# Performance work log

Hardware: AMD Instinct MI355X
Metric: run time of the kernel (lower is better)

The kernel has to match this reference:

```python
import jax, jax.numpy as jnp
import numpy as np

B, S, HID, NH = 4, 2048, 1024, 16
DH = HID // NH  # 64
SCALE = 1.0 / float(np.sqrt(DH))


def _linear_params(key, scale=0.02):
    kw, kb = jax.random.split(key)
    W = jax.random.normal(kw, (HID, HID), dtype=jnp.float32) * scale
    b = jax.random.normal(kb, (HID,), dtype=jnp.float32) * scale
    return W, b


def setup_inputs() -> dict:
    key = jax.random.key(0)
    ks = jax.random.split(key, 9)
    x = jax.random.normal(ks[0], (B, S, HID), dtype=jnp.float32)
    reasoning_mask = jax.random.uniform(ks[1], (B, S, 1, 1), dtype=jnp.float32)
    Wq, bq = _linear_params(ks[2])
    Wk, bk = _linear_params(ks[3])
    Wv, bv = _linear_params(ks[4])
    Wqr, bqr = _linear_params(ks[5])
    Wkr, bkr = _linear_params(ks[6])
    Wo, bo = _linear_params(ks[7])
    return {"x": x, "reasoning_mask": reasoning_mask,
            "Wq": Wq, "bq": bq, "Wk": Wk, "bk": bk, "Wv": Wv, "bv": bv,
            "Wqr": Wqr, "bqr": bqr, "Wkr": Wkr, "bkr": bkr, "Wo": Wo, "bo": bo}


def reference(x, reasoning_mask, Wq, bq, Wk, bk, Wv, bv, Wqr, bqr, Wkr, bkr, Wo, bo):
    # Projections: x @ W + b, then view (B, S, NH, DH)
    def proj(W, b):
        return (jnp.einsum('bsh,hd->bsd', x, W) + b).reshape(B, S, NH, DH)

    q = proj(Wq, bq)
    k = proj(Wk, bk)
    v = proj(Wv, bv)
    q_r = proj(Wqr, bqr)
    k_r = proj(Wkr, bkr)

    # Reasoning-gated blend of standard and reasoning projections
    q = q * (1.0 - reasoning_mask) + q_r * reasoning_mask
    k = k * (1.0 - reasoning_mask) + k_r * reasoning_mask

    # Faithful to source: matmul over the LAST two dims of (B,S,NH,DH),
    # i.e. per-token attention ACROSS HEADS -> scores shape (B,S,NH,NH)
    scores = jnp.einsum('bshd,bsed->bshe', q, k) * SCALE
    attn = jax.nn.softmax(scores, axis=-1)  # dropout is identity at eval
    out = jnp.einsum('bshe,bsed->bshd', attn, v)  # (B,S,NH,DH)

    # Faithful transpose(1,2) + contiguous view to (B, S, HID)
    out = jnp.transpose(out, (0, 2, 1, 3)).reshape(B, -1, HID)
    return jnp.einsum('bsh,hd->bsd', out, Wo) + bo
```

## Files before the change

### kernel.cpp

```cpp
#include <hip/hip_runtime.h>
#include <hip/hip_bf16.h>


typedef __attribute__((ext_vector_type(8))) short short8;
typedef __attribute__((ext_vector_type(4))) short short4v;
typedef __attribute__((ext_vector_type(4))) float f32x4;

#define HID 1024
#define NTOK 8192
#define WT_ELEMS (1024 * 1024)

__device__ __forceinline__ short f2bs(float f) {
  __hip_bfloat16 h = __float2bfloat16(f);
  return *reinterpret_cast<short*>(&h);
}
__device__ __forceinline__ float bs2f(short s) {
  __hip_bfloat16 h;
  *reinterpret_cast<short*>(&h) = s;
  return __bfloat162float(h);
}
__device__ __forceinline__ void gload16(const void* g, void* l) {
  __builtin_amdgcn_global_load_lds(
      (const __attribute__((address_space(1))) void*)g,
      (__attribute__((address_space(3))) void*)l, 16, 0, 0);
}

#define BAR() asm volatile("s_barrier" ::: "memory")
#define VMWAIT(N) asm volatile("s_waitcnt vmcnt(" #N ")" ::: "memory")
#define LGKM0 do { asm volatile("s_waitcnt lgkmcnt(0)" ::: "memory"); \
                   __builtin_amdgcn_sched_barrier(0); } while (0)
#define SCB __builtin_amdgcn_sched_barrier(0)
#define PRIO1 __builtin_amdgcn_s_setprio(1)
#define PRIO0 __builtin_amdgcn_s_setprio(0)
#define MFMA16x16 __builtin_amdgcn_mfma_f32_16x16x32_bf16

__global__ __launch_bounds__(256) void prep_kernel(
    const float* __restrict__ W0, const float* __restrict__ W1,
    const float* __restrict__ W2, const float* __restrict__ W3,
    const float* __restrict__ W4, const float* __restrict__ W5,
    const float* __restrict__ X, short* __restrict__ WT, short* __restrict__ XB)
{
  __shared__ short sT[64][68];
  const int bid = blockIdx.x, tid = threadIdx.x;
  if (bid < 1536) {
    const int z = bid >> 8, rem = bid & 255;
    const float* W = z == 0 ? W0 : z == 1 ? W1 : z == 2 ? W2 : z == 3 ? W3
                   : z == 4 ? W4 : W5;
    short* OUT = WT + (size_t)z * WT_ELEMS;
    const int k0 = (rem & 15) * 64, n0 = (rem >> 4) * 64;
    #pragma unroll
    for (int i = 0; i < 4; i++) {
      const int li = tid + i * 256;
      const int kr = li >> 4, c4 = (li & 15) << 2;
      const f32x4 wv = *reinterpret_cast<const f32x4*>(&W[(size_t)(k0 + kr) * HID + n0 + c4]);
      short4v s4;
      #pragma unroll
      for (int j = 0; j < 4; j++) s4[j] = f2bs(wv[j]);
      *reinterpret_cast<short4v*>(&sT[kr][c4]) = s4;
    }
    __syncthreads();
    #pragma unroll
    for (int i = 0; i < 4; i++) {
      const int li = tid + i * 256;
      const int nr = li >> 4, k4 = (li & 15) << 2;
      short4v o;
      #pragma unroll
      for (int j = 0; j < 4; j++) o[j] = sT[k4 + j][nr];
      const int kcol = (k0 + k4) ^ ((nr & 7) << 3);
      *reinterpret_cast<short4v*>(&OUT[(size_t)(n0 + nr) * HID + kcol]) = o;
    }
  } else {
    const int gid = (bid - 1536) * 256 + tid;
    const int row = gid >> 7, kc = (gid & 127) << 3;
    const f32x4 a = *reinterpret_cast<const f32x4*>(&X[(size_t)row * HID + kc]);
    const f32x4 b = *reinterpret_cast<const f32x4*>(&X[(size_t)row * HID + kc + 4]);
    short8 s;
    #pragma unroll
    for (int j = 0; j < 4; j++) { s[j] = f2bs(a[j]); s[4 + j] = f2bs(b[j]); }
    const int phys = (kc & ~63) | ((kc & 63) ^ ((row & 7) << 3));
    *reinterpret_cast<short8*>(&XB[(size_t)row * HID + phys]) = s;
  }
}

__global__ __launch_bounds__(512, 2) void gated8_kernel(
    const short* __restrict__ XB, const short* __restrict__ WTbase,
    const float* __restrict__ bq, const float* __restrict__ bqr,
    const float* __restrict__ bk, const float* __restrict__ bkr,
    const float* __restrict__ MASK,
    __hip_bfloat16* __restrict__ qg, __hip_bfloat16* __restrict__ kg)
{
  __shared__ short lA[2][256][64];
  __shared__ short lB1[2][128][64];
  __shared__ short lB2[2][128][64];

  const int d = blockIdx.x;
  const int bx = d & 31, byz = d >> 5;
  const int by = byz & 7, z = byz >> 3;

  const short* W1T = WTbase + (size_t)(2 * z) * WT_ELEMS;
  const short* W2T = W1T + WT_ELEMS;
  const float* B1b = z ? bk : bq;
  const float* B2b = z ? bkr : bqr;
  __hip_bfloat16* OUT = z ? kg : qg;

  const int m0 = bx * 256, n0 = by * 128;
  const int tid = threadIdx.x, lane = tid & 63, w = tid >> 6;
  const int wr = (w >> 1) * 64, wc = (w & 1) * 64;
  const int lrow = lane & 15, lkhi = (lane >> 4) << 3;
  const int swz = (lrow & 7) << 3;
  const int srow = lane >> 3, scol = (lane & 7) << 3;

  f32x4 acc1[4][4] = {}, acc2[4][4] = {};
  short8 bf1k[4], bf2k[4];
  short8 afA0, afA1, afA2, afA3;
  short8 afB0, afB1, afB2, afB3;

  auto stA2 = [&](int slot, int kt, int i0) {
    const int k0 = kt * 64;
    #pragma unroll
    for (int i = 0; i < 2; i++) {
      const int chunk = w * 4 + i0 + i;
      gload16(&XB[(size_t)(m0 + chunk * 8 + srow) * HID + k0 + scol],
              &lA[slot][chunk * 8][0]);
    }
  };
  auto stB1s = [&](int slot, int kt) {
    const int k0 = kt * 64;
    #pragma unroll
    for (int i = 0; i < 2; i++) {
      const int chunk = w * 2 + i;
      gload16(&W1T[(size_t)(n0 + chunk * 8 + srow) * HID + k0 + scol],
              &lB1[slot][chunk * 8][0]);
    }
  };
  auto stB2s = [&](int slot, int kt) {
    const int k0 = kt * 64;
    #pragma unroll
    for (int i = 0; i < 2; i++) {
      const int chunk = w * 2 + i;
      gload16(&W2T[(size_t)(n0 + chunk * 8 + srow) * HID + k0 + scol],
              &lB2[slot][chunk * 8][0]);
    }
  };
  auto rdA = [&](int s, int m, int kk) -> short8 {
    const int lk = (kk * 32 + lkhi) ^ swz;
    return *reinterpret_cast<const short8*>(&lA[s][wr + m * 16 + lrow][lk]);
  };

#define RDB1(S, KK)                                                                   \
  _Pragma("unroll")                                                                   \
  for (int n = 0; n < 4; n++) {                                                       \
    const int lk = ((KK) * 32 + lkhi) ^ swz;                                          \
    bf1k[n] = *reinterpret_cast<const short8*>(&lB1[S][wc + n * 16 + lrow][lk]);      \
  }
#define RDB2(S, KK)                                                                   \
  _Pragma("unroll")                                                                   \
  for (int n = 0; n < 4; n++) {                                                       \
    const int lk = ((KK) * 32 + lkhi) ^ swz;                                          \
    bf2k[n] = *reinterpret_cast<const short8*>(&lB2[S][wc + n * 16 + lrow][lk]);      \
  }
#define MM16A(A0, A1, A2, A3)                                             \
  _Pragma("unroll")                                                       \
  for (int n = 0; n < 4; n++) {                                           \
    acc1[0][n] = MFMA16x16(A0, bf1k[n], acc1[0][n], 0, 0, 0);             \
    acc1[1][n] = MFMA16x16(A1, bf1k[n], acc1[1][n], 0, 0, 0);             \
    acc1[2][n] = MFMA16x16(A2, bf1k[n], acc1[2][n], 0, 0, 0);             \
    acc1[3][n] = MFMA16x16(A3, bf1k[n], acc1[3][n], 0, 0, 0);             \
  }
#define MM16B(A0, A1, A2, A3)                                             \
  _Pragma("unroll")                                                       \
  for (int n = 0; n < 4; n++) {                                           \
    acc2[0][n] = MFMA16x16(A0, bf2k[n], acc2[0][n], 0, 0, 0);             \
    acc2[1][n] = MFMA16x16(A1, bf2k[n], acc2[1][n], 0, 0, 0);             \
    acc2[2][n] = MFMA16x16(A2, bf2k[n], acc2[2][n], 0, 0, 0);             \
    acc2[3][n] = MFMA16x16(A3, bf2k[n], acc2[3][n], 0, 0, 0);             \
  }
#define GTILE(S, SN, TS)                                                 \
                                                                 \
  afA0 = rdA(S, 0, 0); afA1 = rdA(S, 1, 0);                              \
  afA2 = rdA(S, 2, 0); afA3 = rdA(S, 3, 0);                              \
  RDB1(S, 0);                                                            \
  stA2(SN, TS, 0); stA2(SN, TS, 2);                                      \
  BAR(); LGKM0;                                                          \
  PRIO1; MM16A(afA0, afA1, afA2, afA3) PRIO0; SCB;                       \
  VMWAIT(4);                                                             \
  BAR();                                                                 \
                                                                 \
  RDB2(S, 0);                                                            \
  stB1s(SN, TS); stB2s(SN, TS);                                          \
  BAR(); LGKM0;                                                          \
  PRIO1; MM16B(afA0, afA1, afA2, afA3) PRIO0; SCB;                       \
  BAR();                                                                 \
                                                                 \
  afB0 = rdA(S, 0, 1); afB1 = rdA(S, 1, 1);                              \
  afB2 = rdA(S, 2, 1); afB3 = rdA(S, 3, 1);                              \
  RDB1(S, 1);                                                            \
  BAR(); LGKM0;                                                          \
  PRIO1; MM16A(afB0, afB1, afB2, afB3) PRIO0; SCB;                       \
  BAR();                                                                 \
                                                                 \
  RDB2(S, 1);                                                            \
  BAR(); LGKM0;                                                          \
  PRIO1; MM16B(afB0, afB1, afB2, afB3) PRIO0; SCB;                       \
  VMWAIT(2);                                                             \
  BAR();

  stA2(0, 0, 0); stA2(0, 0, 2); stB1s(0, 0); stB2s(0, 0);
  VMWAIT(2);
  BAR();

  #pragma unroll 1
  for (int i = 0; i < 16; i++) {
    const int S = i & 1, SN = S ^ 1;
    const int TS = (i < 15) ? i + 1 : 15;
    GTILE(S, SN, TS)
  }
  VMWAIT(0);
#undef GTILE
#undef MM16A
#undef MM16B
#undef RDB1
#undef RDB2

  #pragma unroll
  for (int m = 0; m < 4; m++) {
    const int rbase = m0 + wr + m * 16 + ((lane >> 4) << 2);
    #pragma unroll
    for (int n = 0; n < 4; n++) {
      const int col = n0 + wc + n * 16 + lrow;
      const float bias1 = B1b[col];
      const float bias2 = B2b[col];
      #pragma unroll
      for (int r = 0; r < 4; r++) {
        const int row = rbase + r;
        const float mk = MASK[row];
        const float val = (acc1[m][n][r] + bias1) * (1.f - mk) +
                          (acc2[m][n][r] + bias2) * mk;
        OUT[(size_t)row * HID + col] = __float2bfloat16(val);
      }
    }
  }
}

template<bool OUTF32>
__global__ __launch_bounds__(512, 2) void plain8_kernel(
    const short* __restrict__ A, const short* __restrict__ WT,
    const float* __restrict__ BIAS, void* __restrict__ OUTv)
{
  __shared__ short lA[3][256][64];
  __shared__ short lB[3][128][64];

  const int d = blockIdx.x;
  const int bx = d & 31, by = d >> 5;

  const int m0 = bx * 256, n0 = by * 128;
  const int tid = threadIdx.x, lane = tid & 63, w = tid >> 6;
  const int wr = (w >> 1) * 64, wc = (w & 1) * 64;
  const int lrow = lane & 15, lkhi = (lane >> 4) << 3;
  const int swz = (lrow & 7) << 3;
  const int srow = lane >> 3, scol = (lane & 7) << 3;

  f32x4 acc[4][4] = {};
  short8 paf[2][4], pbf[2][4];

  auto stTrip = [&](int slot, int kt, int t) {
    const int k0 = kt * 64;
    if (t == 0) {
      #pragma unroll
      for (int i = 0; i < 3; i++) {
        const int chunk = w * 4 + i;
        gload16(&A[(size_t)(m0 + chunk * 8 + srow) * HID + k0 + scol],
                &lA[slot][chunk * 8][0]);
      }
    } else {
      const int chunk = w * 4 + 3;
      gload16(&A[(size_t)(m0 + chunk * 8 + srow) * HID + k0 + scol],
              &lA[slot][chunk * 8][0]);
      #pragma unroll
      for (int i = 0; i < 2; i++) {
        const int bchunk = w * 2 + i;
        gload16(&WT[(size_t)(n0 + bchunk * 8 + srow) * HID + k0 + scol],
                &lB[slot][bchunk * 8][0]);
      }
    }
  };

#define RDP(S, KK)                                                                    \
  _Pragma("unroll")                                                                   \
  for (int m = 0; m < 4; m++) {                                                       \
    const int lk = ((KK) * 32 + lkhi) ^ swz;                                          \
    paf[KK][m] = *reinterpret_cast<const short8*>(&lA[S][wr + m * 16 + lrow][lk]);    \
    pbf[KK][m] = *reinterpret_cast<const short8*>(&lB[S][wc + m * 16 + lrow][lk]);    \
  }
#define PMM16(KK)                                                                     \
  _Pragma("unroll")                                                                   \
  for (int m = 0; m < 4; m++)                                                         \
    _Pragma("unroll")                                                                 \
    for (int n = 0; n < 4; n++)                                                       \
      acc[m][n] = MFMA16x16(paf[KK][m], pbf[KK][n], acc[m][n], 0, 0, 0);

  stTrip(0, 0, 0); stTrip(0, 0, 1);
  stTrip(1, 1, 0); stTrip(1, 1, 1);
  VMWAIT(6);
  BAR();

  int s = 0, s2 = 2;
  #pragma unroll 1
  for (int t = 0; t < 16; t++) {
    const int TS = (t < 14) ? t + 2 : 15;
    RDP(s, 0)
    stTrip(s2, TS, 0);
    BAR(); LGKM0;
    PRIO1; PMM16(0) PRIO0; SCB;
    BAR();
    RDP(s, 1)
    stTrip(s2, TS, 1);
    BAR(); LGKM0;
    PRIO1; PMM16(1) PRIO0; SCB;
    VMWAIT(6);
    BAR();
    s = (s == 2) ? 0 : s + 1;
    s2 = (s2 == 2) ? 0 : s2 + 1;
  }
  VMWAIT(0);
#undef PMM16
#undef RDP

  #pragma unroll
  for (int m = 0; m < 4; m++) {
    const int rbase = m0 + wr + m * 16 + ((lane >> 4) << 2);
    #pragma unroll
    for (int n = 0; n < 4; n++) {
      const int col = n0 + wc + n * 16 + lrow;
      const float bias = BIAS[col];
      #pragma unroll
      for (int r = 0; r < 4; r++) {
        const float val = acc[m][n][r] + bias;
        const size_t oidx = (size_t)(rbase + r) * HID + col;
        if (OUTF32) ((float*)OUTv)[oidx] = val;
        else ((__hip_bfloat16*)OUTv)[oidx] = __float2bfloat16(val);
      }
    }
  }
}

__global__ __launch_bounds__(256) void attn_kernel(
    const __hip_bfloat16* __restrict__ Q, const __hip_bfloat16* __restrict__ K,
    const __hip_bfloat16* __restrict__ V, __hip_bfloat16* __restrict__ O)
{
  const int t = blockIdx.x;
  const int b = t >> 11, s = t & 2047;
  __shared__ float sQ[16][68], sK[16][68], sV[16][68];
  __shared__ float sA[16][17];
  const int tid = threadIdx.x;
  const size_t tb = (size_t)t * HID;

  {
    const int h = tid >> 4, d0 = (tid & 15) << 2;
    const int o = (h << 6) + d0;
    const short4v qv = *reinterpret_cast<const short4v*>(&((const short*)Q)[tb + o]);
    const short4v kv = *reinterpret_cast<const short4v*>(&((const short*)K)[tb + o]);
    const short4v vv = *reinterpret_cast<const short4v*>(&((const short*)V)[tb + o]);
    #pragma unroll
    for (int j = 0; j < 4; j++) {
      sQ[h][d0 + j] = bs2f(qv[j]);
      sK[h][d0 + j] = bs2f(kv[j]);
      sV[h][d0 + j] = bs2f(vv[j]);
    }
  }
  __syncthreads();

  const int h = tid >> 4, e = tid & 15;
  float sc = 0.f;
  #pragma unroll
  for (int dd = 0; dd < 64; dd++) sc += sQ[h][dd] * sK[e][dd];
  sc *= 0.125f;

  float mx = sc;
  mx = fmaxf(mx, __shfl_xor(mx, 1));
  mx = fmaxf(mx, __shfl_xor(mx, 2));
  mx = fmaxf(mx, __shfl_xor(mx, 4));
  mx = fmaxf(mx, __shfl_xor(mx, 8));
  const float p = __expf(sc - mx);
  float sm = p;
  sm += __shfl_xor(sm, 1);
  sm += __shfl_xor(sm, 2);
  sm += __shfl_xor(sm, 4);
  sm += __shfl_xor(sm, 8);
  sA[h][e] = p / sm;
  __syncthreads();

  const int row7 = (s >> 4) & 7;
  const size_t ob = ((size_t)b * 2048 + (s >> 4)) * HID + ((size_t)(s & 15) << 6);
  {
    const int hh = tid >> 4, d4 = (tid & 15) << 2;
    f32x4 o = {0.f, 0.f, 0.f, 0.f};
    #pragma unroll
    for (int e2 = 0; e2 < 16; e2++) {
      const float a = sA[hh][e2];
      #pragma unroll
      for (int j = 0; j < 4; j++) o[j] += a * sV[e2][d4 + j];
    }
    short4v ov;
    #pragma unroll
    for (int j = 0; j < 4; j++) ov[j] = f2bs(o[j]);
    *reinterpret_cast<short4v*>(
        &((short*)O)[ob + (size_t)hh * 128 * HID + (d4 ^ (row7 << 3))]) = ov;
  }
}

extern "C" void kernel_launch(void* const* d_in, const int* in_sizes, int n_in,
                              void* d_out, int out_size, void* d_ws, size_t ws_size,
                              hipStream_t stream) {
  (void)in_sizes; (void)n_in; (void)out_size; (void)ws_size;
  const float* x   = (const float*)d_in[0];
  const float* rm  = (const float*)d_in[1];
  const float* Wq  = (const float*)d_in[2];
  const float* bq  = (const float*)d_in[3];
  const float* Wk  = (const float*)d_in[4];
  const float* bk  = (const float*)d_in[5];
  const float* Wv  = (const float*)d_in[6];
  const float* bv  = (const float*)d_in[7];
  const float* Wqr = (const float*)d_in[8];
  const float* bqr = (const float*)d_in[9];
  const float* Wkr = (const float*)d_in[10];
  const float* bkr = (const float*)d_in[11];
  const float* Wo  = (const float*)d_in[12];
  const float* bo  = (const float*)d_in[13];

  char* ws = (char*)d_ws;
  short* wt = (short*)ws;
  __hip_bfloat16* qg = (__hip_bfloat16*)(ws + 12u * 1024 * 1024);
  __hip_bfloat16* vv = (__hip_bfloat16*)(ws + 28u * 1024 * 1024);
  __hip_bfloat16* ar = (__hip_bfloat16*)(ws + 44u * 1024 * 1024);
  short* xb = (short*)d_out;
  __hip_bfloat16* kg = (__hip_bfloat16*)((char*)d_out + 16u * 1024 * 1024);

  prep_kernel<<<dim3(5632), 256, 0, stream>>>(Wq, Wqr, Wk, Wkr, Wv, Wo, x, wt, xb);
  gated8_kernel<<<dim3(512), 512, 0, stream>>>(xb, wt, bq, bqr, bk, bkr, rm, qg, kg);
  plain8_kernel<false><<<dim3(256), 512, 0, stream>>>(xb, wt + (size_t)4 * WT_ELEMS, bv, vv);
  attn_kernel<<<dim3(NTOK), 256, 0, stream>>>(qg, kg, vv, ar);
  plain8_kernel<true><<<dim3(256), 512, 0, stream>>>((const short*)ar,
                                                     wt + (size_t)5 * WT_ELEMS, bo, d_out);
}
```

Measured before the change: 147.1 us.

## Overlap LDS fragment reads with MFMA using partial lgkmcnt waits, drop intra-tile barriers

Restructures the inner loops of the fused Q/K projection GEMM and the generic projection GEMM. All LDS fragment reads for a k-tile are issued up front, and partial lgkmcnt waits let each MFMA group start as soon as its own operands arrive. This replaces the four barrier-separated phases per tile with a single barrier at the end. The QK kernel now waits for all global loads (vmcnt 0) before each tile's barrier, which may serialize global prefetch latency with compute. The extra B-fragment buffer also raises register pressure.

```diff
diff --git a/kernel.cpp b/kernel.cpp
--- a/kernel.cpp
+++ b/kernel.cpp
@@ -27,8 +27,8 @@
 
 #define BAR() asm volatile("s_barrier" ::: "memory")
 #define VMWAIT(N) asm volatile("s_waitcnt vmcnt(" #N ")" ::: "memory")
-#define LGKM0 do { asm volatile("s_waitcnt lgkmcnt(0)" ::: "memory"); \
-                   __builtin_amdgcn_sched_barrier(0); } while (0)
+#define LGKMW(N) do { asm volatile("s_waitcnt lgkmcnt(" #N ")" ::: "memory"); \
+                      __builtin_amdgcn_sched_barrier(0); } while (0)
 #define SCB __builtin_amdgcn_sched_barrier(0)
 #define PRIO1 __builtin_amdgcn_s_setprio(1)
 #define PRIO0 __builtin_amdgcn_s_setprio(0)
@@ -111,7 +111,7 @@
   const int srow = lane >> 3, scol = (lane & 7) << 3;
 
   f32x4 acc1[4][4] = {}, acc2[4][4] = {};
-  short8 bf1k[4], bf2k[4];
+  short8 bf1k[4], bf2k[4], bf1b[4];
   short8 afA0, afA1, afA2, afA3;
   short8 afB0, afB1, afB2, afB3;
 
@@ -147,66 +147,64 @@
     return *reinterpret_cast<const short8*>(&lA[s][wr + m * 16 + lrow][lk]);
   };
 
-#define RDB1(S, KK)                                                                   \
+#define RDB1(DST, S, KK)                                                              \
   _Pragma("unroll")                                                                   \
   for (int n = 0; n < 4; n++) {                                                       \
     const int lk = ((KK) * 32 + lkhi) ^ swz;                                          \
-    bf1k[n] = *reinterpret_cast<const short8*>(&lB1[S][wc + n * 16 + lrow][lk]);      \
-  }
-#define RDB2(S, KK)                                                                   \
+    DST[n] = *reinterpret_cast<const short8*>(&lB1[S][wc + n * 16 + lrow][lk]);       \
+  }
+#define RDB2(DST, S, KK)                                                              \
   _Pragma("unroll")                                                                   \
   for (int n = 0; n < 4; n++) {                                                       \
     const int lk = ((KK) * 32 + lkhi) ^ swz;                                          \
-    bf2k[n] = *reinterpret_cast<const short8*>(&lB2[S][wc + n * 16 + lrow][lk]);      \
-  }
-#define MM16A(A0, A1, A2, A3)                                             \
+    DST[n] = *reinterpret_cast<const short8*>(&lB2[S][wc + n * 16 + lrow][lk]);       \
+  }
+#define MMC1(A0, A1, A2, A3, BF)                                          \
   _Pragma("unroll")                                                       \
   for (int n = 0; n < 4; n++) {                                           \
-    acc1[0][n] = MFMA16x16(A0, bf1k[n], acc1[0][n], 0, 0, 0);             \
-    acc1[1][n] = MFMA16x16(A1, bf1k[n], acc1[1][n], 0, 0, 0);             \
-    acc1[2][n] = MFMA16x16(A2, bf1k[n], acc1[2][n], 0, 0, 0);             \
-    acc1[3][n] = MFMA16x16(A3, bf1k[n], acc1[3][n], 0, 0, 0);             \
-  }
-#define MM16B(A0, A1, A2, A3)                                             \
+    acc1[0][n] = MFMA16x16(A0, BF[n], acc1[0][n], 0, 0, 0);               \
+    acc1[1][n] = MFMA16x16(A1, BF[n], acc1[1][n], 0, 0, 0);               \
+    acc1[2][n] = MFMA16x16(A2, BF[n], acc1[2][n], 0, 0, 0);               \
+    acc1[3][n] = MFMA16x16(A3, BF[n], acc1[3][n], 0, 0, 0);               \
+  }
+#define MMC2(A0, A1, A2, A3, BF)                                          \
   _Pragma("unroll")                                                       \
   for (int n = 0; n < 4; n++) {                                           \
-    acc2[0][n] = MFMA16x16(A0, bf2k[n], acc2[0][n], 0, 0, 0);             \
-    acc2[1][n] = MFMA16x16(A1, bf2k[n], acc2[1][n], 0, 0, 0);             \
-    acc2[2][n] = MFMA16x16(A2, bf2k[n], acc2[2][n], 0, 0, 0);             \
-    acc2[3][n] = MFMA16x16(A3, bf2k[n], acc2[3][n], 0, 0, 0);             \
+    acc2[0][n] = MFMA16x16(A0, BF[n], acc2[0][n], 0, 0, 0);               \
+    acc2[1][n] = MFMA16x16(A1, BF[n], acc2[1][n], 0, 0, 0);               \
+    acc2[2][n] = MFMA16x16(A2, BF[n], acc2[2][n], 0, 0, 0);               \
+    acc2[3][n] = MFMA16x16(A3, BF[n], acc2[3][n], 0, 0, 0);               \
   }
 #define GTILE(S, SN, TS)                                                 \
-                                                                 \
   afA0 = rdA(S, 0, 0); afA1 = rdA(S, 1, 0);                              \
   afA2 = rdA(S, 2, 0); afA3 = rdA(S, 3, 0);                              \
-  RDB1(S, 0);                                                            \
-  stA2(SN, TS, 0); stA2(SN, TS, 2);                                      \
-  BAR(); LGKM0;                                                          \
-  PRIO1; MM16A(afA0, afA1, afA2, afA3) PRIO0; SCB;                       \
-  VMWAIT(4);                                                             \
-  BAR();                                                                 \
-                                                                 \
-  RDB2(S, 0);                                                            \
-  stB1s(SN, TS); stB2s(SN, TS);                                          \
-  BAR(); LGKM0;                                                          \
-  PRIO1; MM16B(afA0, afA1, afA2, afA3) PRIO0; SCB;                       \
-  BAR();                                                                 \
-                                                                 \
+  SCB;                                                                   \
+  RDB1(bf1k, S, 0);                                                      \
+  SCB;                                                                   \
+  RDB2(bf2k, S, 0);                                                      \
+  SCB;                                                                   \
   afB0 = rdA(S, 0, 1); afB1 = rdA(S, 1, 1);                              \
   afB2 = rdA(S, 2, 1); afB3 = rdA(S, 3, 1);                              \
-  RDB1(S, 1);                                                            \
-  BAR(); LGKM0;                                                          \
-  PRIO1; MM16A(afB0, afB1, afB2, afB3) PRIO0; SCB;                       \
-  BAR();                                                                 \
-                                                                 \
-  RDB2(S, 1);                                                            \
-  BAR(); LGKM0;                                                          \
-  PRIO1; MM16B(afB0, afB1, afB2, afB3) PRIO0; SCB;                       \
-  VMWAIT(2);                                                             \
+  SCB;                                                                   \
+  RDB1(bf1b, S, 1);                                                      \
+  SCB;                                                                   \
+  stA2(SN, TS, 0); stA2(SN, TS, 2); stB1s(SN, TS); stB2s(SN, TS);        \
+  SCB;                                                                   \
+  LGKMW(12);                                                             \
+  PRIO1; MMC1(afA0, afA1, afA2, afA3, bf1k) PRIO0; SCB;                  \
+  LGKMW(8);                                                              \
+  PRIO1; MMC2(afA0, afA1, afA2, afA3, bf2k) PRIO0; SCB;                  \
+  RDB2(bf2k, S, 1);                                                      \
+  SCB;                                                                   \
+  LGKMW(4);                                                              \
+  PRIO1; MMC1(afB0, afB1, afB2, afB3, bf1b) PRIO0; SCB;                  \
+  LGKMW(0);                                                              \
+  PRIO1; MMC2(afB0, afB1, afB2, afB3, bf2k) PRIO0; SCB;                  \
+  VMWAIT(0);                                                             \
   BAR();
 
   stA2(0, 0, 0); stA2(0, 0, 2); stB1s(0, 0); stB2s(0, 0);
-  VMWAIT(2);
+  VMWAIT(0);
   BAR();
 
   #pragma unroll 1
@@ -215,10 +213,9 @@
     const int TS = (i < 15) ? i + 1 : 15;
     GTILE(S, SN, TS)
   }
-  VMWAIT(0);
 #undef GTILE
-#undef MM16A
-#undef MM16B
+#undef MMC1
+#undef MMC2
 #undef RDB1
 #undef RDB2
 
@@ -297,7 +294,7 @@
   for (int m = 0; m < 4; m++)                                                         \
     _Pragma("unroll")                                                                 \
     for (int n = 0; n < 4; n++)                                                       \
-      acc[m][n] = MFMA16x16(paf[KK][m], pbf[KK][n], acc[m][n], 0, 0, 0);
+      acc[m][n] = MFMA16x16(paf[KK][m], pbf[KK][n], acc[KK == 0 ? m : m][n], 0, 0, 0);
 
   stTrip(0, 0, 0); stTrip(0, 0, 1);
   stTrip(1, 1, 0); stTrip(1, 1, 1);
@@ -309,20 +306,20 @@
   for (int t = 0; t < 16; t++) {
     const int TS = (t < 14) ? t + 2 : 15;
     RDP(s, 0)
-    stTrip(s2, TS, 0);
-    BAR(); LGKM0;
+    SCB;
+    RDP(s, 1)
+    SCB;
+    stTrip(s2, TS, 0); stTrip(s2, TS, 1);
+    SCB;
+    LGKMW(8);
     PRIO1; PMM16(0) PRIO0; SCB;
-    BAR();
-    RDP(s, 1)
-    stTrip(s2, TS, 1);
-    BAR(); LGKM0;
+    LGKMW(0);
     PRIO1; PMM16(1) PRIO0; SCB;
     VMWAIT(6);
     BAR();
     s = (s == 2) ? 0 : s + 1;
     s2 = (s2 == 2) ? 0 : s2 + 1;
   }
-  VMWAIT(0);
 #undef PMM16
 #undef RDP
 
```

Result: no change. 145.2 us (-1.3%).
